# Kernel tuning notes

Measured on AMD Instinct MI355X. Metric: run time of the kernel, lower is better.

The kernel has to match this reference:

```python
import jax, jax.numpy as jnp
import numpy as np

NEG_BIG = -1e10  # K.switch(A==0, -1e10, 0) mask value
LRELU_ALPHA = 0.2


def setup_inputs() -> dict:
    key = jax.random.key(0)
    kX, kA, kW, kS, kN = jax.random.split(key, 5)
    B, N, F, H, F_ = 4, 2048, 256, 8, 64
    X = jax.random.normal(kX, (B, N, F), dtype=jnp.float32)
    A = jax.random.bernoulli(kA, 0.05, (B, N, N)).astype(jnp.float32)
    eye = jnp.eye(N, dtype=jnp.float32)[None]
    A = jnp.maximum(A, eye)
    W = jax.random.normal(kW, (H, F, F_), dtype=jnp.float32) * 0.05
    a_self = jax.random.normal(kS, (H, F_), dtype=jnp.float32) * 0.05
    a_neigh = jax.random.normal(kN, (H, F_), dtype=jnp.float32) * 0.05
    return {"X": X, "A": A, "W": W, "a_self": a_self, "a_neigh": a_neigh}


def reference(X, A, W, a_self, a_neigh):
    # per-head linear transform, vectorized over heads: [B,H,N,F_]
    h = jnp.einsum('bnf,hfo->bhno', X, W)
    att_s = jnp.einsum('bhno,ho->bhn', h, a_self)    # attn_for_self
    att_n = jnp.einsum('bhno,ho->bhn', h, a_neigh)   # attn_for_neighs
    # broadcast-add -> dense NxN scores per head, LeakyReLU(0.2)
    dense = att_s[:, :, :, None] + att_n[:, :, None, :]          # [B,H,N,N]
    dense = jax.nn.leaky_relu(dense, LRELU_ALPHA)
    mask = jnp.where(A == 0.0, NEG_BIG, 0.0)[:, None, :, :]      # [B,1,N,N]
    attn = jax.nn.softmax(dense + mask, axis=-1)
    # weighted aggregation (dropout is identity at inference / attn_dropout=0)
    out = jnp.einsum('bhnm,bhmo->bhno', attn, h)                 # [B,H,N,F_]
    out = jax.nn.relu(out)                                       # per-head activation (concat mode)
    B, H, N, F_ = out.shape
    return out.transpose(0, 2, 1, 3).reshape(B, N, H * F_)       # concat heads
```

## Files before the change

### kernel.cpp

```cpp
#include <hip/hip_runtime.h>


constexpr int GN  = 2048;
constexpr int GHF = 512;

using sh8    = __attribute__((ext_vector_type(8))) short;
using hf8    = __attribute__((ext_vector_type(8))) _Float16;
using us4g   = __attribute__((ext_vector_type(4))) unsigned short;
using f32x4g = __attribute__((ext_vector_type(4))) float;
using u32x4g = __attribute__((ext_vector_type(4))) unsigned int;
using i32x4g = __attribute__((ext_vector_type(4))) int;

__device__ inline float gat_bf2f(unsigned short u) {
    union { unsigned int i; float f; } c; c.i = ((unsigned int)u) << 16; return c.f;
}
__device__ inline unsigned short gat_f2bf(float f) {
    union { float f; unsigned int i; } c; c.f = f;
    return (unsigned short)((c.i + 0x7fffu + ((c.i >> 16) & 1u)) >> 16);
}
__device__ inline unsigned short gat_f2h(float f) {
    _Float16 h = (_Float16)f;
    union { _Float16 h; unsigned short u; } c; c.h = h; return c.u;
}
__device__ inline float gat_h2f(unsigned short u) {
    union { _Float16 h; unsigned short u; } c; c.u = u; return (float)c.h;
}
__device__ inline int gat_isf32(const float* __restrict__ Aw) {
    float a = Aw[0];
    return (a == 0.0f) || (a == 1.0f);
}
__device__ inline size_t gat_hswz_idx(int o, int j) {
    int jc = j >> 5, quad = (j >> 3) & 3, e = j & 7;
    int lane = quad * 16 + (o & 15);
    return (((size_t)(jc * 4 + (o >> 4))) * 64 + lane) * 8 + e;
}

__global__ void GraphAttention_62981400429165_kernel() {}

constexpr size_t OFF_HS   = 256;
constexpr size_t OFF_ATTS = OFF_HS   + 8388608;
constexpr size_t OFF_EF   = OFF_ATTS + 262144;
constexpr size_t OFF_E5F  = OFF_EF   + 131072;
constexpr size_t OFF_MASK = OFF_E5F  + 131072;
constexpr size_t OFF_MAXN = OFF_MASK + 2097152;

constexpr int LDW = 264;
__global__ __launch_bounds__(256) void k_gemm1(const float* __restrict__ Xraw,
                                               const float* __restrict__ Wraw,
                                               const float* __restrict__ aSraw,
                                               const float* __restrict__ aNraw,
                                               const float* __restrict__ Aw,
                                               unsigned short* __restrict__ hswz,
                                               float* __restrict__ att_s,
                                               unsigned short* __restrict__ Ef,
                                               unsigned short* __restrict__ E5f,
                                               float* __restrict__ maxn_arr,
                                               unsigned char* __restrict__ maskB) {
    int tid = threadIdx.x, blk = blockIdx.x;
    int isf = gat_isf32(Aw);
    if (blk >= 1024) {
        size_t i8 = ((size_t)(blk - 1024) * 256 + tid) * 8;
        unsigned int byte = 0;
        if (isf) {
            f32x4g v0 = *(const f32x4g*)(Aw + i8);
            f32x4g v1 = *(const f32x4g*)(Aw + i8 + 4);
#pragma unroll
            for (int e = 0; e < 4; e++) {
                byte |= (v0[e] != 0.0f ? 1u : 0u) << e;
                byte |= (v1[e] != 0.0f ? 1u : 0u) << (e + 4);
            }
        } else {
            const unsigned short* Au = (const unsigned short*)Aw;
            u32x4g v = *(const u32x4g*)(Au + i8);
#pragma unroll
            for (int w = 0; w < 4; w++) {
                byte |= ((v[w] & 0xffffu) != 0u ? 1u : 0u) << (2 * w);
                byte |= ((v[w] >> 16) != 0u ? 1u : 0u) << (2 * w + 1);
            }
        }
        maskB[i8 >> 3] = (unsigned char)byte;
        return;
    }
    int bh = blk >> 5, it = blk & 31;
    int b = bh >> 3, hh = bh & 7;
#if defined(__gfx950__)
    __shared__ unsigned short SH[64 * LDW];
    int wave = tid >> 6, lane = tid & 63;
    int lrw = lane & 15, quad = lane >> 4;
    for (int i = 0; i < 64; i++) {
        int k = wave * 64 + i;
        unsigned short v;
        if (isf) v = gat_f2bf(Wraw[(size_t)hh * 16384 + k * 64 + lane]);
        else     v = ((const unsigned short*)Wraw)[(size_t)hh * 16384 + k * 64 + lane];
        SH[(k >> 5) * 2048 + (lane >> 4) * 512 + ((k >> 3) & 3) * 128
           + (lane & 15) * 8 + (k & 7)] = v;
    }
    __syncthreads();
    int row0 = it * 64 + wave * 16;
    size_t xbase = ((size_t)(b * GN) + row0 + lrw) * 256;
    f32x4g acc[4] = {};
#pragma unroll 2
    for (int kg = 0; kg < 8; kg++) {
        sh8 a;
        if (isf) {
            const float* xp = Xraw + xbase + kg * 32 + quad * 8;
            f32x4g x0 = *(const f32x4g*)xp;
            f32x4g x1 = *(const f32x4g*)(xp + 4);
            unsigned int w0_, w1_, w2_, w3_;
            asm("v_cvt_pk_bf16_f32 %0, %1, %2" : "=v"(w0_) : "v"(x0[0]), "v"(x0[1]));
            asm("v_cvt_pk_bf16_f32 %0, %1, %2" : "=v"(w1_) : "v"(x0[2]), "v"(x0[3]));
            asm("v_cvt_pk_bf16_f32 %0, %1, %2" : "=v"(w2_) : "v"(x1[0]), "v"(x1[1]));
            asm("v_cvt_pk_bf16_f32 %0, %1, %2" : "=v"(w3_) : "v"(x1[2]), "v"(x1[3]));
            i32x4g aw = {(int)w0_, (int)w1_, (int)w2_, (int)w3_};
            a = *(sh8*)&aw;
        } else {
            a = *(const sh8*)((const unsigned short*)Xraw + xbase + kg * 32 + quad * 8);
        }
        const unsigned short* wp = &SH[kg * 2048 + lane * 8];
        sh8 w0 = *(const sh8*)&wp[0];
        sh8 w1 = *(const sh8*)&wp[512];
        sh8 w2 = *(const sh8*)&wp[1024];
        sh8 w3 = *(const sh8*)&wp[1536];
        acc[0] = __builtin_amdgcn_mfma_f32_16x16x32_bf16(a, w0, acc[0], 0, 0, 0);
        acc[1] = __builtin_amdgcn_mfma_f32_16x16x32_bf16(a, w1, acc[1], 0, 0, 0);
        acc[2] = __builtin_amdgcn_mfma_f32_16x16x32_bf16(a, w2, acc[2], 0, 0, 0);
        acc[3] = __builtin_amdgcn_mfma_f32_16x16x32_bf16(a, w3, acc[3], 0, 0, 0);
    }
    float as_l[4], an_l[4];
#pragma unroll
    for (int ct = 0; ct < 4; ct++) {
        int col = hh * 64 + ct * 16 + lrw;
        as_l[ct] = isf ? aSraw[col] : gat_bf2f(((const unsigned short*)aSraw)[col]);
        an_l[ct] = isf ? aNraw[col] : gat_bf2f(((const unsigned short*)aNraw)[col]);
    }
    float wmax = -3e38f;
#pragma unroll
    for (int r = 0; r < 4; r++) {
        float ps = acc[0][r] * as_l[0] + acc[1][r] * as_l[1]
                 + acc[2][r] * as_l[2] + acc[3][r] * as_l[3];
        float pn = acc[0][r] * an_l[0] + acc[1][r] * an_l[1]
                 + acc[2][r] * an_l[2] + acc[3][r] * an_l[3];
        for (int off = 1; off < 16; off <<= 1) {
            ps += __shfl_xor(ps, off);
            pn += __shfl_xor(pn, off);
        }
        int row = row0 + quad * 4 + r;
        if (lrw == 0) {
            att_s[bh * GN + row] = ps;
            float pnc = fminf(pn, 10.0f);
            Ef[bh * GN + row]  = gat_f2h(__expf(pnc));
            E5f[bh * GN + row] = gat_f2h(__expf(0.2f * pnc));
        }
        wmax = fmaxf(wmax, pn);
    }
    wmax = fmaxf(wmax, __shfl_xor(wmax, 16));
    wmax = fmaxf(wmax, __shfl_xor(wmax, 32));
    if (lane == 0) maxn_arr[((bh << 5) | it) * 4 + wave] = wmax;
    __syncthreads();
    unsigned short* CtT = SH;
#pragma unroll
    for (int ct = 0; ct < 4; ct++) {
        int o = ct * 16 + lrw;
        int nloc = wave * 16 + quad * 4;
        us4g v;
        v[0] = gat_f2h(acc[ct][0]);
        v[1] = gat_f2h(acc[ct][1]);
        v[2] = gat_f2h(acc[ct][2]);
        v[3] = gat_f2h(acc[ct][3]);
        *(us4g*)&CtT[o * LDW + nloc] = v;
    }
    __syncthreads();
#pragma unroll
    for (int k = 0; k < 2; k++) {
        int id = k * 256 + tid;
        int ln = id & 63, t = id >> 6;
        int jc_loc = t >> 2, ct = t & 3;
        int lrw2 = ln & 15, quad2 = ln >> 4;
        int o = ct * 16 + lrw2;
        int nloc = jc_loc * 32 + quad2 * 8;
        sh8 v = *(const sh8*)&CtT[o * LDW + nloc];
        size_t dst = ((((size_t)(bh * 64 + it * 2 + jc_loc)) * 4 + ct) * 64 + ln) * 8;
        *(sh8*)&hswz[dst] = v;
    }
#else
    __shared__ float fm[256];
    float pn_keep = -3e38f;
    if (tid < 64) {
        int row = it * 64 + tid;
        float hrow[64];
        for (int col = 0; col < 64; col++) {
            float sacc = 0.f;
            for (int k = 0; k < 256; k++) {
                float xv = isf ? Xraw[((size_t)(b * GN) + row) * 256 + k]
                               : gat_bf2f(((const unsigned short*)Xraw)[((size_t)(b * GN) + row) * 256 + k]);
                unsigned short wu = isf ? gat_f2bf(Wraw[(size_t)hh * 16384 + k * 64 + col])
                                        : ((const unsigned short*)Wraw)[(size_t)hh * 16384 + k * 64 + col];
                sacc += xv * gat_bf2f(wu);
            }
            hrow[col] = sacc;
        }
        size_t base = (size_t)bh * 64 * GN;
        for (int col = 0; col < 64; col++)
            hswz[base + gat_hswz_idx(col, row)] = gat_f2h(hrow[col]);
        float ps = 0.f, pn = 0.f;
        for (int col = 0; col < 64; col++) {
            float as = isf ? aSraw[hh * 64 + col] : gat_bf2f(((const unsigned short*)aSraw)[hh * 64 + col]);
            float an = isf ? aNraw[hh * 64 + col] : gat_bf2f(((const unsigned short*)aNraw)[hh * 64 + col]);
            ps += hrow[col] * as;
            pn += hrow[col] * an;
        }
        att_s[bh * GN + row] = ps;
        float pnc = fminf(pn, 10.0f);
        Ef[bh * GN + row]  = gat_f2h(__expf(pnc));
        E5f[bh * GN + row] = gat_f2h(__expf(0.2f * pnc));
        pn_keep = pn;
    }
    fm[tid] = pn_keep;
    __syncthreads();
    if (tid == 0) {
        float m = -3e38f;
        for (int q = 0; q < 256; q++) m = fmaxf(m, fm[q]);
        for (int w = 0; w < 4; w++) maxn_arr[((bh << 5) | it) * 4 + w] = m;
    }
#endif
}

__global__ __launch_bounds__(256, 2) void k_attn_av(const unsigned int* __restrict__ mask32,
                                                    const unsigned short* __restrict__ hswz,
                                                    const float* __restrict__ att_s,
                                                    const unsigned short* __restrict__ Ef,
                                                    const unsigned short* __restrict__ E5f,
                                                    const float* __restrict__ maxn_arr,
                                                    const float* __restrict__ Aw,
                                                    void* __restrict__ outv) {
    int blk = blockIdx.x;
    int bh = blk & 31, it = blk >> 5;
    int b = bh >> 3, hh = bh & 7;
    int i0 = it * 64;
    int tid = threadIdx.x;
    int isf = gat_isf32(Aw);
#if defined(__gfx950__)
    int wave = tid >> 6, lane = tid & 63, lrw = lane & 15, quad = lane >> 4;
    int kq = quad * 8;
    int j0 = wave * 512;
    float mxl = -3e38f;
    for (int q = lane; q < 128; q += 64) mxl = fmaxf(mxl, maxn_arr[bh * 128 + q]);
#pragma unroll
    for (int off = 1; off < 64; off <<= 1) mxl = fmaxf(mxl, __shfl_xor(mxl, off));
    float maxn = mxl;
    const unsigned short* hs = hswz + ((size_t)(bh * 64) + wave * 16) * 2048 + lane * 8;
    const unsigned int* Eu  = (const unsigned int*)Ef  + (size_t)bh * 1024;
    const unsigned int* E5u = (const unsigned int*)E5f + (size_t)bh * 1024;
    unsigned int k1p[4], k2p[4];
    const unsigned int* mrf[4];
#pragma unroll
    for (int f = 0; f < 4; f++) {
        int row = i0 + f * 16 + lrw;
        float s = att_s[bh * GN + row];
        float z = s + maxn;
        float c = fmaxf(z, 0.2f * z);
        k1p[f] = (unsigned int)gat_f2h(__expf(s - c)) * 0x00010001u;
        k2p[f] = (unsigned int)gat_f2h(__expf(0.2f * s - c)) * 0x00010001u;
        mrf[f] = mask32 + ((size_t)(b * GN) + row) * 64 + wave * 16;
    }
    f32x4g acc[4][4] = {};
    f32x4g accl[4] = {};
    hf8 ones;
#pragma unroll
    for (int e = 0; e < 8; e++) ones[e] = (_Float16)1.0f;

#pragma unroll 1
    for (int jg = 0; jg < 4; jg++) {
        u32x4g m0 = *(const u32x4g*)&mrf[0][jg * 4];
        u32x4g m1 = *(const u32x4g*)&mrf[1][jg * 4];
        u32x4g m2 = *(const u32x4g*)&mrf[2][jg * 4];
        u32x4g m3 = *(const u32x4g*)&mrf[3][jg * 4];
#pragma unroll
        for (int sj = 0; sj < 4; sj++) {
            int jc = jg * 4 + sj;
            int jh = ((j0 + jc * 32) >> 1) + quad * 4;
            u32x4g Ep  = *(const u32x4g*)&Eu[jh];
            u32x4g E5p = *(const u32x4g*)&E5u[jh];
            const unsigned short* hp = hs + jc * 2048;
            hf8 b0 = *(const hf8*)&hp[0];
            hf8 b1 = *(const hf8*)&hp[512];
            hf8 b2 = *(const hf8*)&hp[1024];
            hf8 b3 = *(const hf8*)&hp[1536];
            unsigned int wfm[4];
            wfm[0] = m0[sj] >> kq;
            wfm[1] = m1[sj] >> kq;
            wfm[2] = m2[sj] >> kq;
            wfm[3] = m3[sj] >> kq;
#pragma unroll
            for (int f = 0; f < 4; f++) {
                i32x4g fa;
#pragma unroll
                for (int pp = 0; pp < 4; pp++) {
                    unsigned int ew = Ep[pp], e5w = E5p[pp];
                    unsigned int a0, a1, mx;
                    asm("v_pk_mul_f16 %0, %1, %2" : "=v"(a0) : "v"(k1p[f]), "v"(ew));
                    asm("v_pk_mul_f16 %0, %1, %2" : "=v"(a1) : "v"(k2p[f]), "v"(e5w));
                    asm("v_pk_max_f16 %0, %1, %2" : "=v"(mx) : "v"(a0), "v"(a1));
                    unsigned int s0 = (unsigned int)__builtin_amdgcn_sbfe((int)wfm[f], 2u * pp, 1u);
                    unsigned int s1 = (unsigned int)__builtin_amdgcn_sbfe((int)wfm[f], 2u * pp + 1u, 1u);
                    fa[pp] = (int)(mx & ((s0 & 0x0000FFFFu) | (s1 & 0xFFFF0000u)));
                }
                hf8 af = *(hf8*)&fa;
                acc[f][0] = __builtin_amdgcn_mfma_f32_16x16x32_f16(af, b0, acc[f][0], 0, 0, 0);
                acc[f][1] = __builtin_amdgcn_mfma_f32_16x16x32_f16(af, b1, acc[f][1], 0, 0, 0);
                acc[f][2] = __builtin_amdgcn_mfma_f32_16x16x32_f16(af, b2, acc[f][2], 0, 0, 0);
                acc[f][3] = __builtin_amdgcn_mfma_f32_16x16x32_f16(af, b3, acc[f][3], 0, 0, 0);
                accl[f]   = __builtin_amdgcn_mfma_f32_16x16x32_f16(af, ones, accl[f], 0, 0, 0);
            }
        }
    }
    __shared__ float lred[4 * 64];
    __shared__ float lsum[64];
    __shared__ float red[4 * 4 * 16 * 17];
    if (lrw == 0) {
#pragma unroll
        for (int f = 0; f < 4; f++)
#pragma unroll
            for (int r = 0; r < 4; r++)
                lred[wave * 64 + f * 16 + quad * 4 + r] = accl[f][r];
    }
    __syncthreads();
    if (tid < 64)
        lsum[tid] = 1.0f / (lred[tid] + lred[64 + tid] + lred[128 + tid] + lred[192 + tid]);
    __syncthreads();
    for (int ct = 0; ct < 4; ct++) {
#pragma unroll
        for (int f = 0; f < 4; f++)
#pragma unroll
            for (int r = 0; r < 4; r++)
                red[((wave * 4 + f) * 16 + quad * 4 + r) * 17 + lrw] = acc[f][ct][r];
        __syncthreads();
#pragma unroll
        for (int k = 0; k < 4; k++) {
            int pos = k * 256 + tid;
            int f = pos >> 8, r16 = (pos >> 4) & 15, c16 = pos & 15;
            int bse = (f * 16 + r16) * 17 + c16;
            float sum = red[bse] + red[bse + 1088] + red[bse + 2176] + red[bse + 3264];
            float v = sum * lsum[f * 16 + r16];
            v = v > 0.f ? v : 0.f;
            int row = i0 + f * 16 + r16;
            size_t o = ((size_t)(b * GN) + row) * GHF + hh * 64 + ct * 16 + c16;
            if (isf) ((float*)outv)[o] = v;
            else     ((unsigned short*)outv)[o] = gat_f2bf(v);
        }
        __syncthreads();
    }
#else
    float maxn = -3e38f;
    for (int q = 0; q < 128; q++) maxn = fmaxf(maxn, maxn_arr[bh * 128 + q]);
    int row = i0 + (tid >> 2), chh = (tid & 3) * 16;
    const unsigned short* hbb = hswz + (size_t)(bh * 64) * GN;
    const unsigned int* mr = mask32 + ((size_t)(b * GN) + row) * 64;
    float s = att_s[bh * GN + row];
    float z = s + maxn;
    float c = fmaxf(z, 0.2f * z);
    unsigned short k1u = gat_f2h(__expf(s - c));
    unsigned short k2u = gat_f2h(__expf(0.2f * s - c));
    float l = 0.f;
    float accS[16] = {};
    for (int j = 0; j < GN; j++) {
        if (!((mr[j >> 5] >> (j & 31)) & 1u)) continue;
        float a0 = gat_h2f(gat_f2h(gat_h2f(k1u) * gat_h2f(Ef[(size_t)bh * GN + j])));
        float a1 = gat_h2f(gat_f2h(gat_h2f(k2u) * gat_h2f(E5f[(size_t)bh * GN + j])));
        float p = fmaxf(a0, a1);
        l += p;
        for (int cc = 0; cc < 16; cc++)
            accS[cc] += p * gat_h2f(hbb[gat_hswz_idx(chh + cc, j)]);
    }
    float li = 1.0f / l;
    for (int cc = 0; cc < 16; cc++) {
        float v = accS[cc] * li; v = v > 0.f ? v : 0.f;
        size_t oi = ((size_t)(b * GN) + row) * GHF + hh * 64 + chh + cc;
        if (isf) ((float*)outv)[oi] = v;
        else     ((unsigned short*)outv)[oi] = gat_f2bf(v);
    }
#endif
}

extern "C" void kernel_launch(void* const* d_in, const int* in_sizes, int n_in,
                              void* d_out, int out_size, void* d_ws, size_t ws_size,
                              hipStream_t stream) {
    const float* X  = (const float*)d_in[0];
    const float* A  = (const float*)d_in[1];
    const float* W  = (const float*)d_in[2];
    const float* aS = (const float*)d_in[3];
    const float* aN = (const float*)d_in[4];

    char* ws = (char*)d_ws;
    unsigned short* hswz = (unsigned short*)(ws + OFF_HS);
    float* att_s = (float*)(ws + OFF_ATTS);
    unsigned short* Ef  = (unsigned short*)(ws + OFF_EF);
    unsigned short* E5f = (unsigned short*)(ws + OFF_E5F);
    unsigned char* maskB = (unsigned char*)(ws + OFF_MASK);
    float* maxn_arr = (float*)(ws + OFF_MAXN);

    k_gemm1<<<9216, 256, 0, stream>>>(X, W, aS, aN, A,
                                      hswz, att_s, Ef, E5f, maxn_arr, maskB);
    k_attn_av<<<1024, 256, 0, stream>>>((const unsigned int*)maskB, hswz,
                                        att_s, Ef, E5f, maxn_arr,
                                        A, d_out);
}
```

Measured before the change: 176.5 us.

## Fuse GEMM, mask packing and attention into one cooperative persistent kernel

Splits the projection GEMM, adjacency-mask packing and attention/aggregation bodies into device helpers. A new cooperative kernel of 512 blocks runs two GEMM units and sixteen mask chunks per block, synchronises the grid, then runs two attention units per block. This removes the second kernel launch and the gap between kernels. In exchange, mask packing and GEMM now run serially per block with much less concurrency, and it relies on cooperative-launch support. If the cooperative launch is unavailable it falls back to the original two-kernel path.

```diff
diff --git a/kernel.cpp b/kernel.cpp
--- a/kernel.cpp
+++ b/kernel.cpp
@@ -1,4 +1,7 @@
 #include <hip/hip_runtime.h>
+#include <hip/hip_cooperative_groups.h>
+
+namespace cg = cooperative_groups;
 
 
 constexpr int GN  = 2048;
@@ -45,48 +48,24 @@
 constexpr size_t OFF_MAXN = OFF_MASK + 2097152;
 
 constexpr int LDW = 264;
-__global__ __launch_bounds__(256) void k_gemm1(const float* __restrict__ Xraw,
-                                               const float* __restrict__ Wraw,
-                                               const float* __restrict__ aSraw,
-                                               const float* __restrict__ aNraw,
-                                               const float* __restrict__ Aw,
-                                               unsigned short* __restrict__ hswz,
-                                               float* __restrict__ att_s,
-                                               unsigned short* __restrict__ Ef,
-                                               unsigned short* __restrict__ E5f,
-                                               float* __restrict__ maxn_arr,
-                                               unsigned char* __restrict__ maskB) {
-    int tid = threadIdx.x, blk = blockIdx.x;
-    int isf = gat_isf32(Aw);
-    if (blk >= 1024) {
-        size_t i8 = ((size_t)(blk - 1024) * 256 + tid) * 8;
-        unsigned int byte = 0;
-        if (isf) {
-            f32x4g v0 = *(const f32x4g*)(Aw + i8);
-            f32x4g v1 = *(const f32x4g*)(Aw + i8 + 4);
-#pragma unroll
-            for (int e = 0; e < 4; e++) {
-                byte |= (v0[e] != 0.0f ? 1u : 0u) << e;
-                byte |= (v1[e] != 0.0f ? 1u : 0u) << (e + 4);
-            }
-        } else {
-            const unsigned short* Au = (const unsigned short*)Aw;
-            u32x4g v = *(const u32x4g*)(Au + i8);
-#pragma unroll
-            for (int w = 0; w < 4; w++) {
-                byte |= ((v[w] & 0xffffu) != 0u ? 1u : 0u) << (2 * w);
-                byte |= ((v[w] >> 16) != 0u ? 1u : 0u) << (2 * w + 1);
-            }
-        }
-        maskB[i8 >> 3] = (unsigned char)byte;
-        return;
-    }
-    int bh = blk >> 5, it = blk & 31;
+
+__device__ inline void gat_gemm_unit(int unit, int tid, int isf,
+                                     const float* __restrict__ Xraw,
+                                     const float* __restrict__ Wraw,
+                                     const float* __restrict__ aSraw,
+                                     const float* __restrict__ aNraw,
+                                     unsigned short* __restrict__ hswz,
+                                     float* __restrict__ att_s,
+                                     unsigned short* __restrict__ Ef,
+                                     unsigned short* __restrict__ E5f,
+                                     float* __restrict__ maxn_arr,
+                                     unsigned short* SH) {
+#if defined(__gfx950__)
+    int bh = unit >> 5, it = unit & 31;
     int b = bh >> 3, hh = bh & 7;
-#if defined(__gfx950__)
-    __shared__ unsigned short SH[64 * LDW];
     int wave = tid >> 6, lane = tid & 63;
     int lrw = lane & 15, quad = lane >> 4;
+    __syncthreads();
     for (int i = 0; i < 64; i++) {
         int k = wave * 64 + i;
         unsigned short v;
@@ -182,64 +161,22 @@
         size_t dst = ((((size_t)(bh * 64 + it * 2 + jc_loc)) * 4 + ct) * 64 + ln) * 8;
         *(sh8*)&hswz[dst] = v;
     }
-#else
-    __shared__ float fm[256];
-    float pn_keep = -3e38f;
-    if (tid < 64) {
-        int row = it * 64 + tid;
-        float hrow[64];
-        for (int col = 0; col < 64; col++) {
-            float sacc = 0.f;
-            for (int k = 0; k < 256; k++) {
-                float xv = isf ? Xraw[((size_t)(b * GN) + row) * 256 + k]
-                               : gat_bf2f(((const unsigned short*)Xraw)[((size_t)(b * GN) + row) * 256 + k]);
-                unsigned short wu = isf ? gat_f2bf(Wraw[(size_t)hh * 16384 + k * 64 + col])
-                                        : ((const unsigned short*)Wraw)[(size_t)hh * 16384 + k * 64 + col];
-                sacc += xv * gat_bf2f(wu);
-            }
-            hrow[col] = sacc;
-        }
-        size_t base = (size_t)bh * 64 * GN;
-        for (int col = 0; col < 64; col++)
-            hswz[base + gat_hswz_idx(col, row)] = gat_f2h(hrow[col]);
-        float ps = 0.f, pn = 0.f;
-        for (int col = 0; col < 64; col++) {
-            float as = isf ? aSraw[hh * 64 + col] : gat_bf2f(((const unsigned short*)aSraw)[hh * 64 + col]);
-            float an = isf ? aNraw[hh * 64 + col] : gat_bf2f(((const unsigned short*)aNraw)[hh * 64 + col]);
-            ps += hrow[col] * as;
-            pn += hrow[col] * an;
-        }
-        att_s[bh * GN + row] = ps;
-        float pnc = fminf(pn, 10.0f);
-        Ef[bh * GN + row]  = gat_f2h(__expf(pnc));
-        E5f[bh * GN + row] = gat_f2h(__expf(0.2f * pnc));
-        pn_keep = pn;
-    }
-    fm[tid] = pn_keep;
-    __syncthreads();
-    if (tid == 0) {
-        float m = -3e38f;
-        for (int q = 0; q < 256; q++) m = fmaxf(m, fm[q]);
-        for (int w = 0; w < 4; w++) maxn_arr[((bh << 5) | it) * 4 + w] = m;
-    }
 #endif
 }
 
-__global__ __launch_bounds__(256, 2) void k_attn_av(const unsigned int* __restrict__ mask32,
-                                                    const unsigned short* __restrict__ hswz,
-                                                    const float* __restrict__ att_s,
-                                                    const unsigned short* __restrict__ Ef,
-                                                    const unsigned short* __restrict__ E5f,
-                                                    const float* __restrict__ maxn_arr,
-                                                    const float* __restrict__ Aw,
-                                                    void* __restrict__ outv) {
-    int blk = blockIdx.x;
-    int bh = blk & 31, it = blk >> 5;
+__device__ inline void gat_attn_unit(int unit, int tid, int isf,
+                                     const unsigned int* __restrict__ mask32,
+                                     const unsigned short* __restrict__ hswz,
+                                     const float* __restrict__ att_s,
+                                     const unsigned short* __restrict__ Ef,
+                                     const unsigned short* __restrict__ E5f,
+                                     const float* __restrict__ maxn_arr,
+                                     void* __restrict__ outv,
+                                     float* SMEMF) {
+#if defined(__gfx950__)
+    int bh = unit >> 5, it = unit & 31;
     int b = bh >> 3, hh = bh & 7;
     int i0 = it * 64;
-    int tid = threadIdx.x;
-    int isf = gat_isf32(Aw);
-#if defined(__gfx950__)
     int wave = tid >> 6, lane = tid & 63, lrw = lane & 15, quad = lane >> 4;
     int kq = quad * 8;
     int j0 = wave * 512;
@@ -314,9 +251,10 @@
             }
         }
     }
-    __shared__ float lred[4 * 64];
-    __shared__ float lsum[64];
-    __shared__ float red[4 * 4 * 16 * 17];
+    float* lred = SMEMF;
+    float* lsum = lred + 256;
+    float* red  = lsum + 64;
+    __syncthreads();
     if (lrw == 0) {
 #pragma unroll
         for (int f = 0; f < 4; f++)
@@ -350,7 +288,118 @@
         }
         __syncthreads();
     }
+#endif
+}
+
+__device__ inline void gat_mask_chunk(size_t chunk, int tid, int isf,
+                                      const float* __restrict__ Aw,
+                                      unsigned char* __restrict__ maskB) {
+    size_t i8 = (chunk * 256 + tid) * 8;
+    unsigned int byte = 0;
+    if (isf) {
+        f32x4g v0 = *(const f32x4g*)(Aw + i8);
+        f32x4g v1 = *(const f32x4g*)(Aw + i8 + 4);
+#pragma unroll
+        for (int e = 0; e < 4; e++) {
+            byte |= (v0[e] != 0.0f ? 1u : 0u) << e;
+            byte |= (v1[e] != 0.0f ? 1u : 0u) << (e + 4);
+        }
+    } else {
+        const unsigned short* Au = (const unsigned short*)Aw;
+        u32x4g v = *(const u32x4g*)(Au + i8);
+#pragma unroll
+        for (int w = 0; w < 4; w++) {
+            byte |= ((v[w] & 0xffffu) != 0u ? 1u : 0u) << (2 * w);
+            byte |= ((v[w] >> 16) != 0u ? 1u : 0u) << (2 * w + 1);
+        }
+    }
+    maskB[i8 >> 3] = (unsigned char)byte;
+}
+
+__global__ __launch_bounds__(256) void k_gemm1(const float* __restrict__ Xraw,
+                                               const float* __restrict__ Wraw,
+                                               const float* __restrict__ aSraw,
+                                               const float* __restrict__ aNraw,
+                                               const float* __restrict__ Aw,
+                                               unsigned short* __restrict__ hswz,
+                                               float* __restrict__ att_s,
+                                               unsigned short* __restrict__ Ef,
+                                               unsigned short* __restrict__ E5f,
+                                               float* __restrict__ maxn_arr,
+                                               unsigned char* __restrict__ maskB) {
+    int tid = threadIdx.x, blk = blockIdx.x;
+    int isf = gat_isf32(Aw);
+    if (blk >= 1024) {
+        gat_mask_chunk((size_t)(blk - 1024), tid, isf, Aw, maskB);
+        return;
+    }
+#if defined(__gfx950__)
+    __shared__ __align__(16) unsigned short SH[64 * LDW];
+    gat_gemm_unit(blk, tid, isf, Xraw, Wraw, aSraw, aNraw,
+                  hswz, att_s, Ef, E5f, maxn_arr, SH);
 #else
+    int bh = blk >> 5, it = blk & 31;
+    int b = bh >> 3, hh = bh & 7;
+    __shared__ float fm[256];
+    float pn_keep = -3e38f;
+    if (tid < 64) {
+        int row = it * 64 + tid;
+        float hrow[64];
+        for (int col = 0; col < 64; col++) {
+            float sacc = 0.f;
+            for (int k = 0; k < 256; k++) {
+                float xv = isf ? Xraw[((size_t)(b * GN) + row) * 256 + k]
+                               : gat_bf2f(((const unsigned short*)Xraw)[((size_t)(b * GN) + row) * 256 + k]);
+                unsigned short wu = isf ? gat_f2bf(Wraw[(size_t)hh * 16384 + k * 64 + col])
+                                        : ((const unsigned short*)Wraw)[(size_t)hh * 16384 + k * 64 + col];
+                sacc += xv * gat_bf2f(wu);
+            }
+            hrow[col] = sacc;
+        }
+        size_t base = (size_t)bh * 64 * GN;
+        for (int col = 0; col < 64; col++)
+            hswz[base + gat_hswz_idx(col, row)] = gat_f2h(hrow[col]);
+        float ps = 0.f, pn = 0.f;
+        for (int col = 0; col < 64; col++) {
+            float as = isf ? aSraw[hh * 64 + col] : gat_bf2f(((const unsigned short*)aSraw)[hh * 64 + col]);
+            float an = isf ? aNraw[hh * 64 + col] : gat_bf2f(((const unsigned short*)aNraw)[hh * 64 + col]);
+            ps += hrow[col] * as;
+            pn += hrow[col] * an;
+        }
+        att_s[bh * GN + row] = ps;
+        float pnc = fminf(pn, 10.0f);
+        Ef[bh * GN + row]  = gat_f2h(__expf(pnc));
+        E5f[bh * GN + row] = gat_f2h(__expf(0.2f * pnc));
+        pn_keep = pn;
+    }
+    fm[tid] = pn_keep;
+    __syncthreads();
+    if (tid == 0) {
+        float m = -3e38f;
+        for (int q = 0; q < 256; q++) m = fmaxf(m, fm[q]);
+        for (int w = 0; w < 4; w++) maxn_arr[((bh << 5) | it) * 4 + w] = m;
+    }
+#endif
+}
+
+__global__ __launch_bounds__(256, 2) void k_attn_av(const unsigned int* __restrict__ mask32,
+                                                    const unsigned short* __restrict__ hswz,
+                                                    const float* __restrict__ att_s,
+                                                    const unsigned short* __restrict__ Ef,
+                                                    const unsigned short* __restrict__ E5f,
+                                                    const float* __restrict__ maxn_arr,
+                                                    const float* __restrict__ Aw,
+                                                    void* __restrict__ outv) {
+    int tid = threadIdx.x, blk = blockIdx.x;
+    int isf = gat_isf32(Aw);
+#if defined(__gfx950__)
+    __shared__ __align__(16) float SMEMF[256 + 64 + 4 * 4 * 16 * 17];
+    gat_attn_unit(blk, tid, isf, mask32, hswz, att_s, Ef, E5f, maxn_arr,
+                  outv, SMEMF);
+#else
+    int bh = blk >> 5, it = blk & 31;
+    int b = bh >> 3, hh = bh & 7;
+    int i0 = it * 64;
     float maxn = -3e38f;
     for (int q = 0; q < 128; q++) maxn = fmaxf(maxn, maxn_arr[bh * 128 + q]);
     int row = i0 + (tid >> 2), chh = (tid & 3) * 16;
@@ -382,6 +431,40 @@
 #endif
 }
 
+__global__ __launch_bounds__(256, 2) void k_fused(const float* __restrict__ Xraw,
+                                                  const float* __restrict__ Wraw,
+                                                  const float* __restrict__ aSraw,
+                                                  const float* __restrict__ aNraw,
+                                                  const float* __restrict__ Aw,
+                                                  unsigned short* __restrict__ hswz,
+                                                  float* __restrict__ att_s,
+                                                  unsigned short* __restrict__ Ef,
+                                                  unsigned short* __restrict__ E5f,
+                                                  float* __restrict__ maxn_arr,
+                                                  unsigned char* __restrict__ maskB,
+                                                  void* __restrict__ outv) {
+    int tid = threadIdx.x, blk = blockIdx.x;
+    int isf = gat_isf32(Aw);
+    __shared__ __align__(16) unsigned char SMEMRAW[64 * LDW * 2];
+
+#if defined(__gfx950__)
+    for (int u = 0; u < 2; u++)
+        gat_gemm_unit(blk * 2 + u, tid, isf, Xraw, Wraw, aSraw, aNraw,
+                      hswz, att_s, Ef, E5f, maxn_arr,
+                      (unsigned short*)SMEMRAW);
+    for (int mc = 0; mc < 16; mc++)
+        gat_mask_chunk((size_t)blk * 16 + mc, tid, isf, Aw, maskB);
+    __threadfence();
+    cg::this_grid().sync();
+    __threadfence();
+    for (int u = 0; u < 2; u++)
+        gat_attn_unit(blk * 2 + u, tid, isf, (const unsigned int*)maskB,
+                      hswz, att_s, Ef, E5f, maxn_arr, outv, (float*)SMEMRAW);
+#else
+    (void)SMEMRAW;
+#endif
+}
+
 extern "C" void kernel_launch(void* const* d_in, const int* in_sizes, int n_in,
                               void* d_out, int out_size, void* d_ws, size_t ws_size,
                               hipStream_t stream) {
@@ -398,10 +481,30 @@
     unsigned short* E5f = (unsigned short*)(ws + OFF_E5F);
     unsigned char* maskB = (unsigned char*)(ws + OFF_MASK);
     float* maxn_arr = (float*)(ws + OFF_MAXN);
-
+    void* outp = d_out;
+
+    static int coop_ok = -1;
+    if (coop_ok < 0) {
+        int dev = 0;
+        (void)hipGetDevice(&dev);
+        int has = 0;
+        (void)hipDeviceGetAttribute(&has, hipDeviceAttributeCooperativeLaunch, dev);
+        int nb = 0;
+        hipError_t qe = hipOccupancyMaxActiveBlocksPerMultiprocessor(&nb, k_fused, 256, 0);
+        coop_ok = (has != 0 && qe == hipSuccess && nb >= 2) ? 1 : 0;
+    }
+
+    if (coop_ok == 1) {
+        void* args[] = {(void*)&X, (void*)&W, (void*)&aS, (void*)&aN, (void*)&A,
+                        (void*)&hswz, (void*)&att_s, (void*)&Ef, (void*)&E5f,
+                        (void*)&maxn_arr, (void*)&maskB, (void*)&outp};
+        hipError_t err = hipLaunchCooperativeKernel((void*)k_fused, dim3(512),
+                                                    dim3(256), args, 0, stream);
+        if (err == hipSuccess) return;
+        coop_ok = 0;
+    }
     k_gemm1<<<9216, 256, 0, stream>>>(X, W, aS, aN, A,
                                       hswz, att_s, Ef, E5f, maxn_arr, maskB);
     k_attn_av<<<1024, 256, 0, stream>>>((const unsigned int*)maskB, hswz,
-                                        att_s, Ef, E5f, maxn_arr,
-                                        A, d_out);
-}
+                                        att_s, Ef, E5f, maxn_arr, A, d_out);
+}
```

Measured after the change: 189.5 us. +7.4%, slower.
